# Optimization experiments

Hardware: AMD Instinct MI355X
Metric: run time of the kernel (lower is better)

## Reference

```python
import jax, jax.numpy as jnp
import numpy as np

INDIM, OUTDIM, K, EXPAND = 256, 256, 3, 64
STRIDE, PAD, DIL, GROUPS = 1, 1, 1, 1


def _make_mask(rng):
    # expander connectivity: indim == outdim, so use the 'else' branch of the
    # torch code: for each input channel, pick EXPAND output channels.
    m = np.zeros((OUTDIM, INDIM), dtype=np.float32)
    for i in range(INDIM):
        x = rng.permutation(OUTDIM)[:EXPAND]
        m[x, i] = 1.0
    # repeat over the kernel spatial dims
    return np.broadcast_to(m[:, :, None, None], (OUTDIM, INDIM, K, K)).copy()


def setup_inputs() -> dict:
    key = jax.random.key(0)
    k1, k2 = jax.random.split(key)
    x = jax.random.normal(k1, (32, INDIM, 56, 56), dtype=jnp.float32)
    # kaiming_normal_(mode='fan_out'): std = sqrt(2 / (outdim * k * k))
    std = np.sqrt(2.0 / (OUTDIM * K * K)).astype(np.float32)
    weight = jax.random.normal(k2, (OUTDIM, INDIM, K, K), dtype=jnp.float32) * std
    mask = jnp.asarray(_make_mask(np.random.default_rng(0)))
    return {"x": x, "weight": weight, "mask": mask}


def reference(x, weight, mask) -> jnp.ndarray:
    w = weight * mask  # zero out non-expander connections
    return jax.lax.conv_general_dilated(
        x, w,
        window_strides=(STRIDE, STRIDE),
        padding=((PAD, PAD), (PAD, PAD)),
        rhs_dilation=(DIL, DIL),
        feature_group_count=GROUPS,
        dimension_numbers=("NCHW", "OIHW", "NCHW"),
    )
```

## Files before the change

### kernel.cpp

```cpp
#include <hip/hip_runtime.h>
#include <hip/hip_bf16.h>

typedef short short8 __attribute__((ext_vector_type(8)));
typedef float float4v __attribute__((ext_vector_type(4)));

#define NIMG 32
#define CIN 256
#define COUT 256
#define HH 56
#define WW 56
#define HP 58
#define WP 58
#define PIXIMG (HH * WW)
#define TOTPIX (NIMG * PIXIMG)
#define OUTSTRIDE_N (COUT * PIXIMG)

static constexpr size_t XT_ELEMS = (size_t)NIMG * HP * WP * CIN;
static constexpr size_t WT_ELEMS = (size_t)9 * COUT * CIN;

static __device__ __forceinline__ unsigned short f2bf(float f) {
    unsigned int u = __builtin_bit_cast(unsigned int, f);
    u = (u + 0x7fffu + ((u >> 16) & 1u)) >> 16;
    return (unsigned short)u;
}

static __device__ __forceinline__ void gl16(const unsigned short* g, char* l) {
    __builtin_amdgcn_global_load_lds(
        (const __attribute__((address_space(1))) void*)g,
        (__attribute__((address_space(3))) void*)l, 16, 0, 0);
}

__global__ __launch_bounds__(256) void k_transpose(const float* __restrict__ x,
                                                   unsigned short* __restrict__ xt) {
    int b   = blockIdx.x;
    int icb = b & 3;
    int h   = (b >> 2) % HH;
    int n   = b / (4 * HH);
    __shared__ __align__(16) char lds[64 * 128];

    int t    = threadIdx.x;
    int w    = t & 63;
    int icl0 = t >> 6;
    if (w < WW) {
        const float* src = x + ((size_t)(n * CIN + icb * 64 + icl0) * HH + h) * WW + w;
#pragma unroll
        for (int j = 0; j < 16; ++j) {
            float v = src[(size_t)(j * 4) * PIXIMG];
            int icl = icl0 + j * 4;
            *(unsigned short*)(lds + w * 128 + ((icl * 2) ^ ((w & 7) << 4))) = f2bf(v);
        }
    }
    __syncthreads();
    int ic4 = t & 15;
    int wr  = t >> 4;
    unsigned short* dst = xt + (size_t)((n * HP + h + 1) * WP + 1) * CIN + icb * 64 + ic4 * 4;
#pragma unroll
    for (int p = 0; p < 4; ++p) {
        int w2 = wr + p * 16;
        if (w2 < WW) {
            uint2 v = *(const uint2*)(lds + w2 * 128 + ((ic4 * 8) ^ ((w2 & 7) << 4)));
            *(uint2*)(dst + (size_t)w2 * CIN) = v;
        }
    }
}

__global__ __launch_bounds__(256) void k_prepw(const float* __restrict__ wgt,
                                               const float* __restrict__ msk,
                                               unsigned short* __restrict__ wt) {
    int t = blockIdx.x * 256 + threadIdx.x;
    const float* wp = wgt + (size_t)t * 9;
    const float* mp = msk + (size_t)t * 9;
#pragma unroll
    for (int tap = 0; tap < 9; ++tap)
        wt[(size_t)tap * (COUT * CIN) + t] = f2bf(wp[tap] * mp[tap]);
}

__global__ __launch_bounds__(256) void k_conv(const unsigned short* __restrict__ xt,
                                              const unsigned short* __restrict__ wt,
                                              float* __restrict__ out) {
    __shared__ __align__(16) char lds[128 * 132 * 4];

    const int t    = threadIdx.x;
    const int lane = t & 63;
    const int wid  = t >> 6;
    const int woc  = wid >> 1;
    const int wpx  = wid & 1;

    const int b0 = blockIdx.x;
    const int b  = (b0 & 7) * 196 + (b0 >> 3);
    const int ptile = b >> 1;
    const int ocb   = b & 1;

    const int srow8 = lane >> 3;
    const int sc    = ((lane & 7) ^ srow8) << 3;

    const unsigned short* aS[4];
    const unsigned short* bS[4];
    char* dA[4];
    char* dB[4];
#pragma unroll
    for (int c = 0; c < 4; ++c) {
        int r = wid * 32 + c * 8 + srow8;
        aS[c] = wt + (size_t)(ocb * 128 + r) * CIN + sc;
        int pg  = ptile * 128 + r;
        int n   = pg / PIXIMG;
        int rem = pg - n * PIXIMG;
        int h   = rem / WW, w = rem - h * WW;
        bS[c] = xt + (size_t)((n * HP + h) * WP + w) * CIN + sc;
        dA[c] = lds + (wid * 32 + c * 8) * 128;
        dB[c] = lds + 16384 + (wid * 32 + c * 8) * 128;
    }

    const int l15  = lane & 15;
    const int lg   = lane >> 4;
    const int swzf = (lane & 7) << 4;
    int colk[2];
    colk[0] = (lg * 16) ^ swzf;
    colk[1] = (64 + lg * 16) ^ swzf;
    int rowA[4], rowB[4];
#pragma unroll
    for (int i = 0; i < 4; ++i) {
        rowA[i] = (woc * 64 + i * 16 + l15) * 128;
        rowB[i] = (wpx * 64 + i * 16 + l15) * 128;
    }

    float4v acc[4][4];
#pragma unroll
    for (int i = 0; i < 4; ++i)
#pragma unroll
        for (int j = 0; j < 4; ++j)
            acc[i][j] = (float4v){0.f, 0.f, 0.f, 0.f};

#define STAGE(BUFOFF, S)                                                     \
    do {                                                                     \
        int tap_ = (S) >> 2, ics_ = (S) & 3;                                 \
        int dh_  = (tap_ * 86) >> 8;                                         \
        int dw_  = tap_ - dh_ * 3;                                           \
        size_t ao_ = (size_t)tap_ * (COUT * CIN) + ics_ * 64;                \
        size_t bo_ = (size_t)(dh_ * WP + dw_) * CIN + ics_ * 64;             \
        _Pragma("unroll")                                                    \
        for (int c_ = 0; c_ < 4; ++c_)                                       \
            gl16(aS[c_] + ao_, dA[c_] + (BUFOFF));                           \
        _Pragma("unroll")                                                    \
        for (int c_ = 0; c_ < 4; ++c_)                                       \
            gl16(bS[c_] + bo_, dB[c_] + (BUFOFF));                           \
    } while (0)

#define COMPUTE(BUFOFF)                                                      \
    do {                                                                     \
        _Pragma("unroll")                                                    \
        for (int kk_ = 0; kk_ < 2; ++kk_) {                                  \
            short8 af_[4], bf_[4];                                           \
            _Pragma("unroll")                                                \
            for (int i_ = 0; i_ < 4; ++i_)                                   \
                af_[i_] = *(const short8*)(lds + (BUFOFF) + rowA[i_] + colk[kk_]); \
            _Pragma("unroll")                                                \
            for (int i_ = 0; i_ < 4; ++i_)                                   \
                bf_[i_] = *(const short8*)(lds + (BUFOFF) + 16384 + rowB[i_] + colk[kk_]); \
            _Pragma("unroll")                                                \
            for (int oi_ = 0; oi_ < 4; ++oi_)                                \
                _Pragma("unroll")                                            \
                for (int pi_ = 0; pi_ < 4; ++pi_)                            \
                    acc[oi_][pi_] = __builtin_amdgcn_mfma_f32_16x16x32_bf16( \
                        af_[oi_], bf_[pi_], acc[oi_][pi_], 0, 0, 0);         \
        }                                                                    \
    } while (0)

    STAGE(0, 0);
    __syncthreads();

#pragma unroll 1
    for (int it = 0; it < 18; ++it) {
        int s1 = 2 * it + 1;
        STAGE(32768, s1);
        COMPUTE(0);
        __syncthreads();
        int s2 = 2 * it + 2;
        if (s2 < 36)
            STAGE(0, s2);
        COMPUTE(32768);
        __syncthreads();
    }
#undef STAGE
#undef COMPUTE

    float* ep = (float*)lds;
#pragma unroll
    for (int oi = 0; oi < 4; ++oi)
#pragma unroll
        for (int pi = 0; pi < 4; ++pi)
#pragma unroll
            for (int r = 0; r < 4; ++r)
                ep[(woc * 64 + oi * 16 + lg * 4 + r) * 132 +
                   (wpx * 64 + pi * 16 + l15)] = acc[oi][pi][r];
    __syncthreads();

    const int rrow = t >> 5;
    const int rcol = (t & 31) * 4;
    {
        int pg  = ptile * 128 + rcol;
        int n   = pg / PIXIMG;
        int rem = pg - n * PIXIMG;
        float* ob = out + (size_t)n * OUTSTRIDE_N + (size_t)(ocb * 128) * PIXIMG + rem;
#pragma unroll
        for (int rd = 0; rd < 16; ++rd) {
            int row = rd * 8 + rrow;
            float4v v = *(const float4v*)&ep[row * 132 + rcol];
            *(float4v*)(ob + (size_t)row * PIXIMG) = v;
        }
    }
}

__global__ __launch_bounds__(256) void k_naive(const float* __restrict__ x,
                                               const float* __restrict__ wg,
                                               const float* __restrict__ mk,
                                               float* __restrict__ out, int total) {
    int idx = blockIdx.x * 256 + threadIdx.x;
    if (idx >= total) return;
    int w  = idx % WW;
    int h  = (idx / WW) % HH;
    int oc = (idx / PIXIMG) % COUT;
    int n  = idx / (COUT * PIXIMG);
    float s = 0.f;
    for (int ic = 0; ic < CIN; ++ic) {
        const float* xp = x + (size_t)(n * CIN + ic) * PIXIMG;
        const float* wp = wg + (size_t)(oc * CIN + ic) * 9;
        const float* mp = mk + (size_t)(oc * CIN + ic) * 9;
#pragma unroll
        for (int kh = 0; kh < 3; ++kh) {
            int hy = h + kh - 1;
            if ((unsigned)hy >= HH) continue;
#pragma unroll
            for (int kw = 0; kw < 3; ++kw) {
                int wx = w + kw - 1;
                if ((unsigned)wx >= WW) continue;
                s += xp[hy * WW + wx] * wp[kh * 3 + kw] * mp[kh * 3 + kw];
            }
        }
    }
    out[idx] = s;
}

extern "C" void kernel_launch(void* const* d_in, const int* in_sizes, int n_in,
                              void* d_out, int out_size, void* d_ws, size_t ws_size,
                              hipStream_t stream) {
    const float* x  = (const float*)d_in[0];
    const float* wg = (const float*)d_in[1];
    const float* mk = (const float*)d_in[2];
    float* out = (float*)d_out;

    size_t need = XT_ELEMS * 2 + WT_ELEMS * 2 + 256;
    if (ws_size < need) {
        int total = NIMG * COUT * PIXIMG;
        k_naive<<<(total + 255) / 256, 256, 0, stream>>>(x, wg, mk, out, total);
        return;
    }

    unsigned short* xt = (unsigned short*)d_ws;
    unsigned short* wt = (unsigned short*)((char*)d_ws + XT_ELEMS * 2);

    hipMemsetAsync(d_ws, 0, XT_ELEMS * 2, stream);
    k_transpose<<<NIMG * HH * 4, 256, 0, stream>>>(x, xt);
    k_prepw<<<(COUT * CIN) / 256, 256, 0, stream>>>(wg, mk, wt);
    k_conv<<<(TOTPIX / 128) * 2, 256, 0, stream>>>(xt, wt, out);
}
```

Measured before the change: 178.7 us.

## Single-buffer conv LDS for occupancy, split epilogue, fuse pad zeroing into transpose

The conv kernel drops its double-buffered LDS pipeline for a single 32KB buffer and sets launch bounds of 3 blocks per CU, trading load/compute overlap for higher occupancy. The epilogue writes output in two 64-row halves so the smaller LDS footprint still fits the transpose staging. The full-workspace memset is removed, and the transpose kernel now zeroes only the padding border rows and columns. Less overlap inside each block may hurt if latency hiding across blocks does not make up for it.

```diff
diff --git a/kernel.cpp b/kernel.cpp
--- a/kernel.cpp
+++ b/kernel.cpp
@@ -34,13 +34,21 @@
                                                    unsigned short* __restrict__ xt) {
     int b   = blockIdx.x;
     int icb = b & 3;
-    int h   = (b >> 2) % HH;
-    int n   = b / (4 * HH);
+    int hp  = (b >> 2) % HP;
+    int n   = b / (4 * HP);
+    unsigned short* rowb = xt + ((size_t)(n * HP + hp) * WP) * CIN + icb * 64;
+    int t = threadIdx.x;
+
+    if (hp == 0 || hp == HP - 1) {
+        for (int idx = t; idx < WP * 8; idx += 256) {
+            int wq = idx >> 3, q = idx & 7;
+            *(uint4*)(rowb + (size_t)wq * CIN + q * 8) = (uint4){0, 0, 0, 0};
+        }
+        return;
+    }
+    int h = hp - 1;
     __shared__ __align__(16) char lds[64 * 128];
-
-    int t    = threadIdx.x;
-    int w    = t & 63;
-    int icl0 = t >> 6;
+    int w = t & 63, icl0 = t >> 6;
     if (w < WW) {
         const float* src = x + ((size_t)(n * CIN + icb * 64 + icl0) * HH + h) * WW + w;
 #pragma unroll
@@ -51,9 +59,8 @@
         }
     }
     __syncthreads();
-    int ic4 = t & 15;
-    int wr  = t >> 4;
-    unsigned short* dst = xt + (size_t)((n * HP + h + 1) * WP + 1) * CIN + icb * 64 + ic4 * 4;
+    int ic4 = t & 15, wr = t >> 4;
+    unsigned short* dst = rowb + (size_t)CIN + ic4 * 4;
 #pragma unroll
     for (int p = 0; p < 4; ++p) {
         int w2 = wr + p * 16;
@@ -61,6 +68,10 @@
             uint2 v = *(const uint2*)(lds + w2 * 128 + ((ic4 * 8) ^ ((w2 & 7) << 4)));
             *(uint2*)(dst + (size_t)w2 * CIN) = v;
         }
+    }
+    if (t < 32) {
+        int col = (t >> 4) * (WP - 1);
+        *(uint2*)(rowb + (size_t)col * CIN + (t & 15) * 4) = (uint2){0, 0};
     }
 }
 
@@ -75,10 +86,10 @@
         wt[(size_t)tap * (COUT * CIN) + t] = f2bf(wp[tap] * mp[tap]);
 }
 
-__global__ __launch_bounds__(256) void k_conv(const unsigned short* __restrict__ xt,
-                                              const unsigned short* __restrict__ wt,
-                                              float* __restrict__ out) {
-    __shared__ __align__(16) char lds[128 * 132 * 4];
+__global__ __launch_bounds__(256, 3) void k_conv(const unsigned short* __restrict__ xt,
+                                                 const unsigned short* __restrict__ wt,
+                                                 float* __restrict__ out) {
+    __shared__ __align__(16) char lds[64 * 132 * 4];
 
     const int t    = threadIdx.x;
     const int lane = t & 63;
@@ -91,22 +102,21 @@
     const int ptile = b >> 1;
     const int ocb   = b & 1;
 
-    const int srow8 = lane >> 3;
-    const int sc    = ((lane & 7) ^ srow8) << 3;
-
+    const int rl  = lane >> 3;
+    const int sc  = ((lane & 7) ^ rl) * 8;
     const unsigned short* aS[4];
     const unsigned short* bS[4];
     char* dA[4];
     char* dB[4];
 #pragma unroll
     for (int c = 0; c < 4; ++c) {
-        int r = wid * 32 + c * 8 + srow8;
+        int r = wid * 32 + c * 8 + rl;
         aS[c] = wt + (size_t)(ocb * 128 + r) * CIN + sc;
         int pg  = ptile * 128 + r;
         int n   = pg / PIXIMG;
         int rem = pg - n * PIXIMG;
         int h   = rem / WW, w = rem - h * WW;
-        bS[c] = xt + (size_t)((n * HP + h) * WP + w) * CIN + sc;
+        bS[c] = xt + ((size_t)((n * HP + h) * WP + w)) * CIN + sc;
         dA[c] = lds + (wid * 32 + c * 8) * 128;
         dB[c] = lds + 16384 + (wid * 32 + c * 8) * 128;
     }
@@ -121,7 +131,7 @@
 #pragma unroll
     for (int i = 0; i < 4; ++i) {
         rowA[i] = (woc * 64 + i * 16 + l15) * 128;
-        rowB[i] = (wpx * 64 + i * 16 + l15) * 128;
+        rowB[i] = 16384 + (wpx * 64 + i * 16 + l15) * 128;
     }
 
     float4v acc[4][4];
@@ -131,83 +141,65 @@
         for (int j = 0; j < 4; ++j)
             acc[i][j] = (float4v){0.f, 0.f, 0.f, 0.f};
 
-#define STAGE(BUFOFF, S)                                                     \
-    do {                                                                     \
-        int tap_ = (S) >> 2, ics_ = (S) & 3;                                 \
-        int dh_  = (tap_ * 86) >> 8;                                         \
-        int dw_  = tap_ - dh_ * 3;                                           \
-        size_t ao_ = (size_t)tap_ * (COUT * CIN) + ics_ * 64;                \
-        size_t bo_ = (size_t)(dh_ * WP + dw_) * CIN + ics_ * 64;             \
-        _Pragma("unroll")                                                    \
-        for (int c_ = 0; c_ < 4; ++c_)                                       \
-            gl16(aS[c_] + ao_, dA[c_] + (BUFOFF));                           \
-        _Pragma("unroll")                                                    \
-        for (int c_ = 0; c_ < 4; ++c_)                                       \
-            gl16(bS[c_] + bo_, dB[c_] + (BUFOFF));                           \
-    } while (0)
-
-#define COMPUTE(BUFOFF)                                                      \
-    do {                                                                     \
-        _Pragma("unroll")                                                    \
-        for (int kk_ = 0; kk_ < 2; ++kk_) {                                  \
-            short8 af_[4], bf_[4];                                           \
-            _Pragma("unroll")                                                \
-            for (int i_ = 0; i_ < 4; ++i_)                                   \
-                af_[i_] = *(const short8*)(lds + (BUFOFF) + rowA[i_] + colk[kk_]); \
-            _Pragma("unroll")                                                \
-            for (int i_ = 0; i_ < 4; ++i_)                                   \
-                bf_[i_] = *(const short8*)(lds + (BUFOFF) + 16384 + rowB[i_] + colk[kk_]); \
-            _Pragma("unroll")                                                \
-            for (int oi_ = 0; oi_ < 4; ++oi_)                                \
-                _Pragma("unroll")                                            \
-                for (int pi_ = 0; pi_ < 4; ++pi_)                            \
-                    acc[oi_][pi_] = __builtin_amdgcn_mfma_f32_16x16x32_bf16( \
-                        af_[oi_], bf_[pi_], acc[oi_][pi_], 0, 0, 0);         \
-        }                                                                    \
-    } while (0)
-
-    STAGE(0, 0);
-    __syncthreads();
-
 #pragma unroll 1
-    for (int it = 0; it < 18; ++it) {
-        int s1 = 2 * it + 1;
-        STAGE(32768, s1);
-        COMPUTE(0);
-        __syncthreads();
-        int s2 = 2 * it + 2;
-        if (s2 < 36)
-            STAGE(0, s2);
-        COMPUTE(32768);
-        __syncthreads();
-    }
-#undef STAGE
-#undef COMPUTE
+    for (int s = 0; s < 36; ++s) {
+        const int tap = s >> 2;
+        const int dh  = (tap * 86) >> 8;
+        const int dw  = tap - dh * 3;
+        const size_t ao = (size_t)tap * (COUT * CIN) + (size_t)((s & 3) << 6);
+        const size_t bo = (size_t)(dh * WP + dw) * CIN + (size_t)((s & 3) << 6);
+#pragma unroll
+        for (int c = 0; c < 4; ++c) gl16(aS[c] + ao, dA[c]);
+#pragma unroll
+        for (int c = 0; c < 4; ++c) gl16(bS[c] + bo, dB[c]);
+        __syncthreads();
+#pragma unroll
+        for (int kk = 0; kk < 2; ++kk) {
+            short8 af[4], bfr[4];
+#pragma unroll
+            for (int i = 0; i < 4; ++i)
+                af[i] = *(const short8*)(lds + rowA[i] + colk[kk]);
+#pragma unroll
+            for (int i = 0; i < 4; ++i)
+                bfr[i] = *(const short8*)(lds + rowB[i] + colk[kk]);
+#pragma unroll
+            for (int oi = 0; oi < 4; ++oi)
+#pragma unroll
+                for (int pi = 0; pi < 4; ++pi)
+                    acc[oi][pi] = __builtin_amdgcn_mfma_f32_16x16x32_bf16(
+                        af[oi], bfr[pi], acc[oi][pi], 0, 0, 0);
+        }
+        __syncthreads();
+    }
 
     float* ep = (float*)lds;
-#pragma unroll
-    for (int oi = 0; oi < 4; ++oi)
-#pragma unroll
-        for (int pi = 0; pi < 4; ++pi)
-#pragma unroll
-            for (int r = 0; r < 4; ++r)
-                ep[(woc * 64 + oi * 16 + lg * 4 + r) * 132 +
-                   (wpx * 64 + pi * 16 + l15)] = acc[oi][pi][r];
-    __syncthreads();
-
-    const int rrow = t >> 5;
-    const int rcol = (t & 31) * 4;
-    {
+#pragma unroll 1
+    for (int c = 0; c < 2; ++c) {
+        if (woc == c) {
+#pragma unroll
+            for (int oi = 0; oi < 4; ++oi)
+#pragma unroll
+                for (int pi = 0; pi < 4; ++pi)
+#pragma unroll
+                    for (int r = 0; r < 4; ++r)
+                        ep[(oi * 16 + lg * 4 + r) * 132 +
+                           (wpx * 64 + pi * 16 + l15)] = acc[oi][pi][r];
+        }
+        __syncthreads();
+        const int rrow = t >> 5;
+        const int rcol = (t & 31) * 4;
         int pg  = ptile * 128 + rcol;
-        int n   = pg / PIXIMG;
-        int rem = pg - n * PIXIMG;
-        float* ob = out + (size_t)n * OUTSTRIDE_N + (size_t)(ocb * 128) * PIXIMG + rem;
-#pragma unroll
-        for (int rd = 0; rd < 16; ++rd) {
+        int n2  = pg / PIXIMG;
+        int rem = pg - n2 * PIXIMG;
+        float* ob = out + (size_t)n2 * OUTSTRIDE_N +
+                    (size_t)(ocb * 128 + c * 64) * PIXIMG + rem;
+#pragma unroll
+        for (int rd = 0; rd < 8; ++rd) {
             int row = rd * 8 + rrow;
             float4v v = *(const float4v*)&ep[row * 132 + rcol];
             *(float4v*)(ob + (size_t)row * PIXIMG) = v;
         }
+        __syncthreads();
     }
 }
 
@@ -259,8 +251,7 @@
     unsigned short* xt = (unsigned short*)d_ws;
     unsigned short* wt = (unsigned short*)((char*)d_ws + XT_ELEMS * 2);
 
-    hipMemsetAsync(d_ws, 0, XT_ELEMS * 2, stream);
-    k_transpose<<<NIMG * HH * 4, 256, 0, stream>>>(x, xt);
+    k_transpose<<<NIMG * HP * 4, 256, 0, stream>>>(x, xt);
     k_prepw<<<(COUT * CIN) / 256, 256, 0, stream>>>(wg, mk, wt);
     k_conv<<<(TOTPIX / 128) * 2, 256, 0, stream>>>(xt, wt, out);
 }
```

After: 152.5 us. 1.17x faster.
